# Kernel optimization log

Hardware: AMD Instinct MI355X
Metric: run time of the kernel (lower is better)

The kernel has to match this reference:

```python
import jax, jax.numpy as jnp
import numpy as np

NUM_HEADS = 8
EPS = 1e-5


def setup_inputs() -> dict:
    key = jax.random.key(0)
    k1, k2, k3 = jax.random.split(key, 3)
    C = 512
    x = jax.random.normal(k1, (16, C, 32, 32), dtype=jnp.float32)
    # 1x1 conv1d weights stored as [out, in] (kernel size 1 squeezed)
    w_qkv = jax.random.normal(k2, (3 * C, C), dtype=jnp.float32) * (1.0 / np.sqrt(C))
    b_qkv = jnp.zeros((3 * C,), dtype=jnp.float32)
    w_proj = jax.random.normal(k3, (C, C), dtype=jnp.float32) * (1.0 / np.sqrt(C))
    b_proj = jnp.zeros((C,), dtype=jnp.float32)
    return {"x": x, "w_qkv": w_qkv, "b_qkv": b_qkv, "w_proj": w_proj, "b_proj": b_proj}


def reference(x, w_qkv, b_qkv, w_proj, b_proj):
    b, c, H, W = x.shape
    T = H * W
    xf = x.reshape(b, c, T)
    # z_normalize over spatial dim (dim 2..) per (batch, channel), biased var
    mean = jnp.mean(xf, axis=2, keepdims=True)
    var = jnp.var(xf, axis=2, keepdims=True)
    xn = (xf - mean) / jnp.sqrt(var + EPS)
    # 1x1 conv: qkv projection -> [b, 3c, T]
    qkv = jnp.einsum('oc,bct->bot', w_qkv, xn) + b_qkv[None, :, None]
    ch = c // NUM_HEADS
    # legacy layout: [b, H*3*C, T] -> [b*H, 3*ch, T] -> split
    qkv = qkv.reshape(b * NUM_HEADS, 3 * ch, T)
    q, k, v = qkv[:, :ch], qkv[:, ch:2 * ch], qkv[:, 2 * ch:]
    scale = 1.0 / np.sqrt(np.sqrt(ch)).astype(np.float32)
    weight = jnp.einsum('bct,bcs->bts', q * scale, k * scale)  # [b*H, T, T]
    weight = jax.nn.softmax(weight.astype(jnp.float32), axis=-1).astype(q.dtype)
    a = jnp.einsum('bts,bcs->bct', weight, v).reshape(b, c, T)
    h = jnp.einsum('oc,bct->bot', w_proj, a) + b_proj[None, :, None]
    return (xn + h).reshape(b, c, H, W)
```

## Files before the change

kernel.cpp:

```cpp
#include <hip/hip_runtime.h>
#include <hip/hip_bf16.h>

using bf16x8s = __attribute__((ext_vector_type(8))) short;
using f32x4   = __attribute__((ext_vector_type(4))) float;
using f32x16  = __attribute__((ext_vector_type(16))) float;
using u32x4   = __attribute__((ext_vector_type(4))) unsigned int;

#define DEVI __device__ __forceinline__

static constexpr int BB  = 16;
static constexpr int CC  = 512;
static constexpr int TT  = 1024;
static constexpr int OQ  = 1536;
static constexpr int NH  = 8;
static constexpr int CHD = 64;

DEVI void load_lds16(const void* g, void* l) {
  __builtin_amdgcn_global_load_lds((const __attribute__((address_space(1))) void*)g,
                                   (__attribute__((address_space(3))) void*)l,
                                   16, 0, 0);
}

DEVI unsigned int cvtpk_bf16(float lo, float hi) {
  unsigned int r;
  asm("v_cvt_pk_bf16_f32 %0, %1, %2" : "=v"(r) : "v"(lo), "v"(hi));
  return r;
}

DEVI float fexp2(float x) {
  float r;
  asm("v_exp_f32 %0, %1" : "=v"(r) : "v"(x));
  return r;
}

DEVI void plswap(unsigned int a, unsigned int b, unsigned int& x, unsigned int& y) {
#if __has_builtin(__builtin_amdgcn_permlane32_swap)
  auto r = __builtin_amdgcn_permlane32_swap((int)a, (int)b, false, false);
  x = (unsigned int)r[0];
  y = (unsigned int)r[1];
#else
  unsigned int pa = (unsigned int)__shfl_xor((int)a, 32);
  unsigned int pb = (unsigned int)__shfl_xor((int)b, 32);
  const bool hi = (threadIdx.x & 32) != 0;
  x = hi ? pb : a;
  y = hi ? b : pa;
#endif
}

__global__ __launch_bounds__(256) void k_convert_w(const float* __restrict__ wq,
                                                   const float* __restrict__ wp,
                                                   __hip_bfloat16* __restrict__ wqb,
                                                   __hip_bfloat16* __restrict__ wpb) {
  int i = blockIdx.x * 256 + threadIdx.x;
  const int NQ = OQ * CC;
  if (i < NQ) wqb[i] = __float2bfloat16(wq[i]);
  else        wpb[i - NQ] = __float2bfloat16(wp[i - NQ]);
}

__global__ __launch_bounds__(256) void k_ln_stats(const float* __restrict__ x,
                                                  float* __restrict__ mean,
                                                  float* __restrict__ rstd) {
  const int row = blockIdx.x;
  const float4* xv = (const float4*)(x + (size_t)row * TT);
  float4 v = xv[threadIdx.x];
  float s = v.x + v.y + v.z + v.w;
  float q = v.x * v.x + v.y * v.y + v.z * v.z + v.w * v.w;
  #pragma unroll
  for (int off = 1; off < 64; off <<= 1) {
    s += __shfl_xor(s, off);
    q += __shfl_xor(q, off);
  }
  __shared__ float ss[4], sq[4];
  const int wave = threadIdx.x >> 6;
  if ((threadIdx.x & 63) == 0) { ss[wave] = s; sq[wave] = q; }
  __syncthreads();
  if (threadIdx.x == 0) {
    float S = ss[0] + ss[1] + ss[2] + ss[3];
    float Q = sq[0] + sq[1] + sq[2] + sq[3];
    float m = S * (1.0f / TT);
    float var = Q * (1.0f / TT) - m * m;
    mean[row] = m;
    rstd[row] = 1.0f / sqrtf(var + 1e-5f);
  }
}

__global__ __launch_bounds__(256) void k_normT(const float* __restrict__ x,
                                               const float* __restrict__ mean,
                                               const float* __restrict__ rstd,
                                               __hip_bfloat16* __restrict__ xnT) {
  const int t0 = blockIdx.x * 64;
  const int c0 = blockIdx.y * 64;
  const int b  = blockIdx.z;
  __shared__ __hip_bfloat16 tile[64][66];
  const int tl = threadIdx.x & 63;
  const int cb = (threadIdx.x >> 6) * 16;
  #pragma unroll
  for (int i = 0; i < 16; ++i) {
    const int cl = cb + i;
    const int gc = b * CC + c0 + cl;
    float v = x[(size_t)gc * TT + t0 + tl];
    float xn = (v - mean[gc]) * rstd[gc];
    tile[tl][cl] = __float2bfloat16(xn);
  }
  __syncthreads();
  #pragma unroll
  for (int i = 0; i < 16; ++i) {
    const int tl2 = cb + i;
    const int cl2 = tl;
    xnT[((size_t)(b * TT + t0 + tl2)) * CC + c0 + cl2] = tile[tl2][cl2];
  }
}

__global__ __launch_bounds__(256) void k_qkv_gemm(const __hip_bfloat16* __restrict__ Wq,
                                                  const __hip_bfloat16* __restrict__ Xt,
                                                  const float* __restrict__ bias,
                                                  __hip_bfloat16* __restrict__ Qb,
                                                  __hip_bfloat16* __restrict__ Kb,
                                                  __hip_bfloat16* __restrict__ Vb) {
  __shared__ __hip_bfloat16 S[2][128 * 64];
  const int tid  = threadIdx.x;
  const int lane = tid & 63;
  const int wave = tid >> 6;
  const int wr = wave >> 1, wc = wave & 1;
  const int tn0 = blockIdx.x * 128;
  const int om0 = blockIdx.y * 128;
  const int b   = blockIdx.z;

  const __hip_bfloat16* Ab  = Wq + (size_t)om0 * CC;
  const __hip_bfloat16* Bbp = Xt + ((size_t)b * TT + tn0) * CC;

  f32x4 acc[4][4] = {};
  const int l15  = lane & 15;
  const int kgrp = (lane >> 4) << 3;

  for (int k0 = 0; k0 < CC; k0 += 64) {
    #pragma unroll
    for (int r = 0; r < 4; ++r) {
      int idx = r * 256 + tid;
      int row = idx >> 3, ch = (idx & 7) << 3;
      load_lds16(Ab + (size_t)row * CC + k0 + ch, &S[0][(r * 256 + wave * 64) * 8]);
    }
    #pragma unroll
    for (int r = 0; r < 4; ++r) {
      int idx = r * 256 + tid;
      int row = idx >> 3, ch = (idx & 7) << 3;
      load_lds16(Bbp + (size_t)row * CC + k0 + ch, &S[1][(r * 256 + wave * 64) * 8]);
    }
    __syncthreads();
    #pragma unroll
    for (int kk = 0; kk < 2; ++kk) {
      const int klo = kk * 32 + kgrp;
      bf16x8s af[4], bfr[4];
      #pragma unroll
      for (int mf = 0; mf < 4; ++mf)
        af[mf] = *(const bf16x8s*)&S[0][(wr * 64 + mf * 16 + l15) * 64 + klo];
      #pragma unroll
      for (int nf = 0; nf < 4; ++nf)
        bfr[nf] = *(const bf16x8s*)&S[1][(wc * 64 + nf * 16 + l15) * 64 + klo];
      #pragma unroll
      for (int mf = 0; mf < 4; ++mf)
        #pragma unroll
        for (int nf = 0; nf < 4; ++nf)
          acc[mf][nf] = __builtin_amdgcn_mfma_f32_16x16x32_bf16(af[mf], bfr[nf], acc[mf][nf], 0, 0, 0);
    }
    __syncthreads();
  }

  const int rg  = (lane >> 4) << 2;
  const int k0c = (om0 >> 6) % 3;
  const int myKind = (wr == 0) ? k0c : (k0c + 1) % 3;
  const int oc  = om0 + wr * 64;
  const int bh  = b * NH + oc / 192;
  const int vwr = (k0c == 2) ? 0 : (((k0c + 1) % 3 == 2) ? 1 : -1);
  __hip_bfloat16* Vt = &S[0][0];

  if (myKind == 2) {
    #pragma unroll
    for (int mf = 0; mf < 4; ++mf)
      #pragma unroll
      for (int j = 0; j < 4; ++j) {
        const int d = mf * 16 + rg + j;
        const float bv = bias[oc + d];
        #pragma unroll
        for (int nf = 0; nf < 4; ++nf) {
          const int tl = wc * 64 + nf * 16 + l15;
          Vt[d * 136 + tl] = __float2bfloat16(acc[mf][nf][j] + bv);
        }
      }
  } else {
    const float qs = (myKind == 0) ? 0.18033688f : 1.0f;
    __hip_bfloat16* outB = (myKind == 0) ? Qb : Kb;
    #pragma unroll
    for (int mf = 0; mf < 4; ++mf) {
      const float b0 = bias[oc + mf * 16 + rg + 0];
      const float b1 = bias[oc + mf * 16 + rg + 1];
      const float b2 = bias[oc + mf * 16 + rg + 2];
      const float b3 = bias[oc + mf * 16 + rg + 3];
      #pragma unroll
      for (int nf = 0; nf < 4; ++nf) {
        const int t = tn0 + wc * 64 + nf * 16 + l15;
        unsigned int lo = cvtpk_bf16((acc[mf][nf][0] + b0) * qs, (acc[mf][nf][1] + b1) * qs);
        unsigned int hi = cvtpk_bf16((acc[mf][nf][2] + b2) * qs, (acc[mf][nf][3] + b3) * qs);
        *(uint2*)&outB[((size_t)bh * TT + t) * CHD + mf * 16 + rg] = make_uint2(lo, hi);
      }
    }
  }

  if (vwr >= 0) {
    __syncthreads();
    const int bhv = b * NH + (om0 + vwr * 64) / 192;
    const int d   = tid >> 2;
    const int tc  = (tid & 3) * 32;
    const __hip_bfloat16* src = Vt + d * 136 + tc;
    __hip_bfloat16* dst = Vb + ((size_t)bhv * CHD + d) * TT + tn0 + tc;
    #pragma unroll
    for (int i = 0; i < 4; ++i)
      *(uint4*)(dst + 8 * i) = *(const uint4*)(src + 8 * i);
  }
}

__global__ __launch_bounds__(256) void k_attn(const __hip_bfloat16* __restrict__ Qb,
                                              const __hip_bfloat16* __restrict__ Kb,
                                              const __hip_bfloat16* __restrict__ Vb,
                                              __hip_bfloat16* __restrict__ aT) {
  const int lane = threadIdx.x & 63;
  const int wave = threadIdx.x >> 6;
  const int bh   = blockIdx.x & 127;
  const int qt   = blockIdx.x >> 7;
  const int q0   = qt * 128 + wave * 32;
  const int l31  = lane & 31;
  const int hi8  = (lane >> 5) << 3;

  __shared__ char lds[2][16384];

  const __hip_bfloat16* Qh = Qb + (size_t)bh * TT * CHD;
  const char* Khc = (const char*)(Kb + (size_t)bh * TT * CHD);
  const char* Vhc = (const char*)(Vb + (size_t)bh * CHD * TT);

  int kO[2], vO[2], dK[2];
  #pragma unroll
  for (int i = 0; i < 2; ++i) {
    const int slot = wave * 128 + i * 64 + lane;
    const int o = slot * 16;
    const int r = o >> 7;
    const int swc = (o & 127) ^ ((r & 7) << 4);
    kO[i] = (o & ~127) + swc;
    vO[i] = r * 2048 + swc;
    dK[i] = (wave * 128 + i * 64) * 16;
  }
  auto stage_to = [&](char* bufp, int kv0) {
    #pragma unroll
    for (int i = 0; i < 2; ++i) {
      load_lds16(Khc + kv0 * 128 + kO[i], bufp + dK[i]);
      load_lds16(Vhc + kv0 * 2  + vO[i], bufp + 8192 + dK[i]);
    }
  };

  bf16x8s aq[4];
  #pragma unroll
  for (int d = 0; d < 4; ++d)
    aq[d] = *(const bf16x8s*)&Qh[(size_t)(q0 + l31) * CHD + d * 16 + hi8];

  f32x16 oacc0 = {}, oacc1 = {};
  float m_run = -1e30f, l_run = 0.f;

  const int sw = (l31 & 7) << 4;
  const int cb = hi8 * 2;

  stage_to(lds[0], 0);
  __syncthreads();

  auto body = [&](int st, const char* kb, const char* vb, char* nbuf, bool do_stage) {
    if (do_stage) stage_to(nbuf, (st + 1) * 64);

    bf16x8s kf0[4], kf1[4];
    #pragma unroll
    for (int d = 0; d < 4; ++d) {
      const int col = d * 32 + cb;
      kf0[d] = *(const bf16x8s*)(kb + l31 * 128        + (col ^ sw));
      kf1[d] = *(const bf16x8s*)(kb + (32 + l31) * 128 + (col ^ sw));
    }

    f32x16 s0 = {}, s1 = {};
    __builtin_amdgcn_s_setprio(1);
    #pragma unroll
    for (int d = 0; d < 4; ++d) {
      s0 = __builtin_amdgcn_mfma_f32_32x32x16_bf16(kf0[d], aq[d], s0, 0, 0, 0);
      s1 = __builtin_amdgcn_mfma_f32_32x32x16_bf16(kf1[d], aq[d], s1, 0, 0, 0);
    }
    __builtin_amdgcn_s_setprio(0);

    bf16x8s vf0[4], vf1[4];
    #pragma unroll
    for (int ks = 0; ks < 4; ++ks) {
      const int col = ks * 32 + cb;
      vf0[ks] = *(const bf16x8s*)(vb + l31 * 128        + (col ^ sw));
      vf1[ks] = *(const bf16x8s*)(vb + (32 + l31) * 128 + (col ^ sw));
    }

    float t16[16];
    #pragma unroll
    for (int i = 0; i < 16; ++i) t16[i] = fmaxf(s0[i], s1[i]);
    float t8[8];
    #pragma unroll
    for (int i = 0; i < 8; ++i) t8[i] = fmaxf(t16[i], t16[i + 8]);
    float t4[4];
    #pragma unroll
    for (int i = 0; i < 4; ++i) t4[i] = fmaxf(t8[i], t8[i + 4]);
    float lmax = fmaxf(fmaxf(t4[0], t4[1]), fmaxf(t4[2], t4[3]));
    float pmax = fmaxf(lmax, __shfl_xor(lmax, 32));

    if (!__all(pmax <= m_run + 11.5f)) {
      const float mnew  = fmaxf(m_run, pmax);
      const float alpha = fexp2(m_run - mnew);
      m_run = mnew;
      l_run *= alpha;
      #pragma unroll
      for (int i = 0; i < 16; ++i) { oacc0[i] *= alpha; oacc1[i] *= alpha; }
    }

    #pragma unroll
    for (int i = 0; i < 16; ++i) s0[i] = fexp2(s0[i] - m_run);
    #pragma unroll
    for (int i = 0; i < 16; ++i) s1[i] = fexp2(s1[i] - m_run);

    unsigned int wa[8], wb[8];
    #pragma unroll
    for (int g = 0; g < 4; ++g) {
      wa[g]     = cvtpk_bf16(s0[4 * g + 0], s0[4 * g + 1]);
      wb[g]     = cvtpk_bf16(s0[4 * g + 2], s0[4 * g + 3]);
      wa[g + 4] = cvtpk_bf16(s1[4 * g + 0], s1[4 * g + 1]);
      wb[g + 4] = cvtpk_bf16(s1[4 * g + 2], s1[4 * g + 3]);
    }

    __builtin_amdgcn_s_setprio(1);
    #pragma unroll
    for (int ks = 0; ks < 4; ++ks) {
      unsigned int x0, y0, x1, y1;
      plswap(wa[2 * ks], wa[2 * ks + 1], x0, y0);
      plswap(wb[2 * ks], wb[2 * ks + 1], x1, y1);
      bf16x8s pf = __builtin_bit_cast(bf16x8s, (u32x4){x0, x1, y0, y1});
      oacc0 = __builtin_amdgcn_mfma_f32_32x32x16_bf16(vf0[ks], pf, oacc0, 0, 0, 0);
      oacc1 = __builtin_amdgcn_mfma_f32_32x32x16_bf16(vf1[ks], pf, oacc1, 0, 0, 0);
    }
    __builtin_amdgcn_s_setprio(0);

    float a8[8];
    #pragma unroll
    for (int i = 0; i < 8; ++i) a8[i] = (s0[i] + s0[i + 8]) + (s1[i] + s1[i + 8]);
    float a4[4];
    #pragma unroll
    for (int i = 0; i < 4; ++i) a4[i] = a8[i] + a8[i + 4];
    float lsum = (a4[0] + a4[1]) + (a4[2] + a4[3]);
    lsum += __shfl_xor(lsum, 32);
    l_run += lsum;

    __syncthreads();
  };

  #pragma unroll 1
  for (int st2 = 0; st2 < 16; st2 += 2) {
    body(st2,     lds[0], lds[0] + 8192, lds[1], true);
    body(st2 + 1, lds[1], lds[1] + 8192, lds[0], st2 + 1 < 15);
  }

  const int b = bh >> 3, h = bh & 7;
  const float rl = 1.0f / l_run;
  const int t = q0 + l31;
  __hip_bfloat16* arow = aT + ((size_t)(b * TT + t)) * CC + h * CHD;
  const int hi4 = hi8 >> 1;
  #pragma unroll
  for (int rr = 0; rr < 4; ++rr) {
    {
      const int c0 = rr * 8 + hi4;
      unsigned int lo = cvtpk_bf16(oacc0[4 * rr + 0] * rl, oacc0[4 * rr + 1] * rl);
      unsigned int hw = cvtpk_bf16(oacc0[4 * rr + 2] * rl, oacc0[4 * rr + 3] * rl);
      *(uint2*)&arow[c0] = make_uint2(lo, hw);
    }
    {
      const int c0 = 32 + rr * 8 + hi4;
      unsigned int lo = cvtpk_bf16(oacc1[4 * rr + 0] * rl, oacc1[4 * rr + 1] * rl);
      unsigned int hw = cvtpk_bf16(oacc1[4 * rr + 2] * rl, oacc1[4 * rr + 3] * rl);
      *(uint2*)&arow[c0] = make_uint2(lo, hw);
    }
  }
}

__global__ __launch_bounds__(256) void k_proj_gemm(const __hip_bfloat16* __restrict__ Wp,
                                                   const __hip_bfloat16* __restrict__ At,
                                                   const float* __restrict__ bias,
                                                   const float* __restrict__ x,
                                                   const float* __restrict__ mean,
                                                   const float* __restrict__ rstd,
                                                   float* __restrict__ out) {
  __shared__ __hip_bfloat16 As2[2][128 * 32];
  __shared__ __hip_bfloat16 Bs2[2][128 * 32];
  const int tid  = threadIdx.x;
  const int lane = tid & 63;
  const int wave = tid >> 6;
  const int wr = wave >> 1, wc = wave & 1;
  const int tn0 = blockIdx.x * 128;
  const int om0 = blockIdx.y * 128;
  const int b   = blockIdx.z;

  const char* Ab  = (const char*)(Wp + (size_t)om0 * CC);
  const char* Bbp = (const char*)(At + ((size_t)b * TT + tn0) * CC);

  f32x4 acc[4][4] = {};
  const int l15  = lane & 15;
  const int frc  = ((lane >> 4) << 3) * 2;
  const int rsw  = ((l15 >> 1) & 3) << 4;

  int srow[2], scsw[2], sdst[2];
  #pragma unroll
  for (int i = 0; i < 2; ++i) {
    const int o = (i * 256 + tid) * 16;
    const int r = o >> 6, c = o & 63;
    srow[i] = r;
    scsw[i] = c ^ (((r >> 1) & 3) << 4);
    sdst[i] = (i * 256 + wave * 64) * 16;
  }

  auto stage = [&](int buf, int k0) {
    const int kb = k0 * 2;
    #pragma unroll
    for (int i = 0; i < 2; ++i) {
      load_lds16(Ab  + (size_t)srow[i] * 1024 + kb + scsw[i], (char*)As2[buf] + sdst[i]);
      load_lds16(Bbp + (size_t)srow[i] * 1024 + kb + scsw[i], (char*)Bs2[buf] + sdst[i]);
    }
  };

  stage(0, 0);
  __syncthreads();

  for (int kt = 0; kt < 16; ++kt) {
    const int buf = kt & 1;
    if (kt < 15) stage(buf ^ 1, (kt + 1) * 32);

    const char* Asb = (const char*)As2[buf];
    const char* Bsb = (const char*)Bs2[buf];
    bf16x8s af[4], bfr[4];
    #pragma unroll
    for (int mf = 0; mf < 4; ++mf)
      af[mf] = *(const bf16x8s*)(Asb + (wr * 64 + mf * 16 + l15) * 64 + (frc ^ rsw));
    #pragma unroll
    for (int nf = 0; nf < 4; ++nf)
      bfr[nf] = *(const bf16x8s*)(Bsb + (wc * 64 + nf * 16 + l15) * 64 + (frc ^ rsw));
    #pragma unroll
    for (int mf = 0; mf < 4; ++mf)
      #pragma unroll
      for (int nf = 0; nf < 4; ++nf)
        acc[mf][nf] = __builtin_amdgcn_mfma_f32_16x16x32_bf16(af[mf], bfr[nf], acc[mf][nf], 0, 0, 0);

    __syncthreads();
  }

  const int rg = (lane >> 4) << 2;
  #pragma unroll
  for (int mf = 0; mf < 4; ++mf) {
    #pragma unroll
    for (int j = 0; j < 4; ++j) {
      const int o = om0 + wr * 64 + mf * 16 + rg + j;
      const int gco = b * CC + o;
      const float bv = bias[o];
      const float mu = mean[gco], rs = rstd[gco];
      #pragma unroll
      for (int nf = 0; nf < 4; ++nf) {
        const int t = tn0 + wc * 64 + nf * 16 + l15;
        const size_t xi = (size_t)gco * TT + t;
        float xn = (x[xi] - mu) * rs;
        out[xi] = xn + acc[mf][nf][j] + bv;
      }
    }
  }
}

extern "C" void kernel_launch(void* const* d_in, const int* in_sizes, int n_in,
                              void* d_out, int out_size, void* d_ws, size_t ws_size,
                              hipStream_t stream) {
  const float* x  = (const float*)d_in[0];
  const float* wq = (const float*)d_in[1];
  const float* bq = (const float*)d_in[2];
  const float* wp = (const float*)d_in[3];
  const float* bp = (const float*)d_in[4];
  float* out = (float*)d_out;

  char* ws = (char*)d_ws;
  __hip_bfloat16* wqb = (__hip_bfloat16*)(ws);
  __hip_bfloat16* wpb = (__hip_bfloat16*)(ws + 1572864);
  float*          mean = (float*)(ws + 2097152);
  float*          rstd = (float*)(ws + 2129920);
  __hip_bfloat16* xnT = (__hip_bfloat16*)(ws + 2162688);
  __hip_bfloat16* Qb  = (__hip_bfloat16*)(ws + 18939904);
  __hip_bfloat16* Kb  = (__hip_bfloat16*)(ws + 35717120);
  __hip_bfloat16* Vb  = (__hip_bfloat16*)(ws + 52494336);
  __hip_bfloat16* aT  = xnT;

  k_convert_w<<<4096, 256, 0, stream>>>(wq, wp, wqb, wpb);
  k_ln_stats<<<BB * CC, 256, 0, stream>>>(x, mean, rstd);
  k_normT<<<dim3(TT / 64, CC / 64, BB), 256, 0, stream>>>(x, mean, rstd, xnT);
  k_qkv_gemm<<<dim3(TT / 128, OQ / 128, BB), 256, 0, stream>>>(wqb, xnT, bq, Qb, Kb, Vb);
  k_attn<<<1024, 256, 0, stream>>>(Qb, Kb, Vb, aT);
  k_proj_gemm<<<dim3(TT / 128, CC / 128, BB), 256, 0, stream>>>(wpb, aT, bp, x, mean, rstd, out);
}
```

Measured before the change: 224.6 us.

## Fuse LN stats and normalize-transpose; restructure attention KV staging loop

Merges the per-row statistics kernel and the normalize-transpose kernel into one kernel, where each block computes stats for 64 channels and then transposes all 1024 timesteps. This removes a launch and the global round-trip of mean/rstd. The catch is that the grid shrinks to only 128 blocks, which may underfill the GPU. In attention, the hand-unrolled two-buffer body is replaced by a plain loop with recomputed staging offsets, and the row-sum reduction is moved before the PV MFMAs.

```diff
diff --git a/kernel.cpp b/kernel.cpp
--- a/kernel.cpp
+++ b/kernel.cpp
@@ -57,57 +57,64 @@
   else        wpb[i - NQ] = __float2bfloat16(wp[i - NQ]);
 }
 
-__global__ __launch_bounds__(256) void k_ln_stats(const float* __restrict__ x,
+__global__ __launch_bounds__(256) void k_ln_fused(const float* __restrict__ x,
                                                   float* __restrict__ mean,
-                                                  float* __restrict__ rstd) {
-  const int row = blockIdx.x;
-  const float4* xv = (const float4*)(x + (size_t)row * TT);
-  float4 v = xv[threadIdx.x];
-  float s = v.x + v.y + v.z + v.w;
-  float q = v.x * v.x + v.y * v.y + v.z * v.z + v.w * v.w;
-  #pragma unroll
-  for (int off = 1; off < 64; off <<= 1) {
-    s += __shfl_xor(s, off);
-    q += __shfl_xor(q, off);
-  }
-  __shared__ float ss[4], sq[4];
-  const int wave = threadIdx.x >> 6;
-  if ((threadIdx.x & 63) == 0) { ss[wave] = s; sq[wave] = q; }
+                                                  float* __restrict__ rstd,
+                                                  __hip_bfloat16* __restrict__ xnT) {
+  const int c0 = blockIdx.x * 64;
+  const int b  = blockIdx.y;
+  const int tid  = threadIdx.x;
+  const int lane = tid & 63;
+  const int wv   = tid >> 6;
+
+  __shared__ float smean[64], srstd[64];
+  __shared__ __hip_bfloat16 tile[64][66];
+
+  #pragma unroll 1
+  for (int k = 0; k < 16; ++k) {
+    const int cl = wv * 16 + k;
+    const int gc = b * CC + c0 + cl;
+    const float4* xr = (const float4*)(x + (size_t)gc * TT);
+    float s = 0.f, q = 0.f;
+    #pragma unroll
+    for (int it = 0; it < 4; ++it) {
+      float4 v = xr[lane + it * 64];
+      s += v.x + v.y + v.z + v.w;
+      q += v.x * v.x + v.y * v.y + v.z * v.z + v.w * v.w;
+    }
+    #pragma unroll
+    for (int off = 1; off < 64; off <<= 1) {
+      s += __shfl_xor(s, off);
+      q += __shfl_xor(q, off);
+    }
+    if (lane == 0) {
+      const float m  = s * (1.0f / TT);
+      const float vr = q * (1.0f / TT) - m * m;
+      const float rs = 1.0f / sqrtf(vr + 1e-5f);
+      smean[cl] = m;  srstd[cl] = rs;
+      mean[gc]  = m;  rstd[gc]  = rs;
+    }
+  }
   __syncthreads();
-  if (threadIdx.x == 0) {
-    float S = ss[0] + ss[1] + ss[2] + ss[3];
-    float Q = sq[0] + sq[1] + sq[2] + sq[3];
-    float m = S * (1.0f / TT);
-    float var = Q * (1.0f / TT) - m * m;
-    mean[row] = m;
-    rstd[row] = 1.0f / sqrtf(var + 1e-5f);
-  }
-}
-
-__global__ __launch_bounds__(256) void k_normT(const float* __restrict__ x,
-                                               const float* __restrict__ mean,
-                                               const float* __restrict__ rstd,
-                                               __hip_bfloat16* __restrict__ xnT) {
-  const int t0 = blockIdx.x * 64;
-  const int c0 = blockIdx.y * 64;
-  const int b  = blockIdx.z;
-  __shared__ __hip_bfloat16 tile[64][66];
-  const int tl = threadIdx.x & 63;
-  const int cb = (threadIdx.x >> 6) * 16;
-  #pragma unroll
-  for (int i = 0; i < 16; ++i) {
-    const int cl = cb + i;
-    const int gc = b * CC + c0 + cl;
-    float v = x[(size_t)gc * TT + t0 + tl];
-    float xn = (v - mean[gc]) * rstd[gc];
-    tile[tl][cl] = __float2bfloat16(xn);
-  }
-  __syncthreads();
-  #pragma unroll
-  for (int i = 0; i < 16; ++i) {
-    const int tl2 = cb + i;
-    const int cl2 = tl;
-    xnT[((size_t)(b * TT + t0 + tl2)) * CC + c0 + cl2] = tile[tl2][cl2];
+
+  const int tl = lane;
+  const int cb = wv * 16;
+  #pragma unroll 1
+  for (int tt = 0; tt < 16; ++tt) {
+    const int t0 = tt * 64;
+    #pragma unroll
+    for (int i = 0; i < 16; ++i) {
+      const int cl = cb + i;
+      const float v = x[(size_t)(b * CC + c0 + cl) * TT + t0 + tl];
+      tile[tl][cl] = __float2bfloat16((v - smean[cl]) * srstd[cl]);
+    }
+    __syncthreads();
+    #pragma unroll
+    for (int i = 0; i < 16; ++i) {
+      const int tl2 = cb + i;
+      xnT[((size_t)(b * TT + t0 + tl2)) * CC + c0 + tl] = tile[tl2][tl];
+    }
+    __syncthreads();
   }
 }
 
@@ -234,25 +241,21 @@
   __shared__ char lds[2][16384];
 
   const __hip_bfloat16* Qh = Qb + (size_t)bh * TT * CHD;
-  const char* Khc = (const char*)(Kb + (size_t)bh * TT * CHD);
-  const char* Vhc = (const char*)(Vb + (size_t)bh * CHD * TT);
-
-  int kO[2], vO[2], dK[2];
-  #pragma unroll
-  for (int i = 0; i < 2; ++i) {
-    const int slot = wave * 128 + i * 64 + lane;
-    const int o = slot * 16;
-    const int r = o >> 7;
-    const int swc = (o & 127) ^ ((r & 7) << 4);
-    kO[i] = (o & ~127) + swc;
-    vO[i] = r * 2048 + swc;
-    dK[i] = (wave * 128 + i * 64) * 16;
-  }
-  auto stage_to = [&](char* bufp, int kv0) {
+  const __hip_bfloat16* Kh = Kb + (size_t)bh * TT * CHD;
+  const __hip_bfloat16* Vh = Vb + (size_t)bh * CHD * TT;
+
+  auto stage = [&](int buf, int kv0) {
+    const char* kg = (const char*)(Kh + (size_t)kv0 * CHD);
+    const char* vg = (const char*)Vh + (size_t)kv0 * 2;
     #pragma unroll
     for (int i = 0; i < 2; ++i) {
-      load_lds16(Khc + kv0 * 128 + kO[i], bufp + dK[i]);
-      load_lds16(Vhc + kv0 * 2  + vO[i], bufp + 8192 + dK[i]);
+      const int slot = wave * 128 + i * 64 + lane;
+      const int o = slot * 16;
+      const int r = o >> 7;
+      const int cs = o & 127;
+      const int swc = cs ^ ((r & 7) << 4);
+      load_lds16(kg + (o & ~127) + swc, &lds[buf][(wave * 128 + i * 64) * 16]);
+      load_lds16(vg + r * 2048 + swc,   &lds[buf][8192 + (wave * 128 + i * 64) * 16]);
     }
   };
 
@@ -267,11 +270,15 @@
   const int sw = (l31 & 7) << 4;
   const int cb = hi8 * 2;
 
-  stage_to(lds[0], 0);
+  stage(0, 0);
   __syncthreads();
 
-  auto body = [&](int st, const char* kb, const char* vb, char* nbuf, bool do_stage) {
-    if (do_stage) stage_to(nbuf, (st + 1) * 64);
+  for (int st = 0; st < 16; ++st) {
+    const int buf = st & 1;
+    if (st < 15) stage(buf ^ 1, (st + 1) * 64);
+
+    const char* kb = lds[buf];
+    const char* vb = lds[buf] + 8192;
 
     bf16x8s kf0[4], kf1[4];
     #pragma unroll
@@ -323,6 +330,15 @@
     for (int i = 0; i < 16; ++i) s0[i] = fexp2(s0[i] - m_run);
     #pragma unroll
     for (int i = 0; i < 16; ++i) s1[i] = fexp2(s1[i] - m_run);
+    float a8[8];
+    #pragma unroll
+    for (int i = 0; i < 8; ++i) a8[i] = (s0[i] + s0[i + 8]) + (s1[i] + s1[i + 8]);
+    float a4[4];
+    #pragma unroll
+    for (int i = 0; i < 4; ++i) a4[i] = a8[i] + a8[i + 4];
+    float lsum = (a4[0] + a4[1]) + (a4[2] + a4[3]);
+    lsum += __shfl_xor(lsum, 32);
+    l_run += lsum;
 
     unsigned int wa[8], wb[8];
     #pragma unroll
@@ -345,23 +361,7 @@
     }
     __builtin_amdgcn_s_setprio(0);
 
-    float a8[8];
-    #pragma unroll
-    for (int i = 0; i < 8; ++i) a8[i] = (s0[i] + s0[i + 8]) + (s1[i] + s1[i + 8]);
-    float a4[4];
-    #pragma unroll
-    for (int i = 0; i < 4; ++i) a4[i] = a8[i] + a8[i + 4];
-    float lsum = (a4[0] + a4[1]) + (a4[2] + a4[3]);
-    lsum += __shfl_xor(lsum, 32);
-    l_run += lsum;
-
-    __syncthreads();
-  };
-
-  #pragma unroll 1
-  for (int st2 = 0; st2 < 16; st2 += 2) {
-    body(st2,     lds[0], lds[0] + 8192, lds[1], true);
-    body(st2 + 1, lds[1], lds[1] + 8192, lds[0], st2 + 1 < 15);
+    __syncthreads();
   }
 
   const int b = bh >> 3, h = bh & 7;
@@ -497,8 +497,7 @@
   __hip_bfloat16* aT  = xnT;
 
   k_convert_w<<<4096, 256, 0, stream>>>(wq, wp, wqb, wpb);
-  k_ln_stats<<<BB * CC, 256, 0, stream>>>(x, mean, rstd);
-  k_normT<<<dim3(TT / 64, CC / 64, BB), 256, 0, stream>>>(x, mean, rstd, xnT);
+  k_ln_fused<<<dim3(CC / 64, BB), 256, 0, stream>>>(x, mean, rstd, xnT);
   k_qkv_gemm<<<dim3(TT / 128, OQ / 128, BB), 256, 0, stream>>>(wqb, xnT, bq, Qb, Kb, Vb);
   k_attn<<<1024, 256, 0, stream>>>(Qb, Kb, Vb, aT);
   k_proj_gemm<<<dim3(TT / 128, CC / 128, BB), 256, 0, stream>>>(wpb, aT, bp, x, mean, rstd, out);
```

After: 249.9 us. 11.3% more time.
